# Optimization experiments

Hardware: AMD Instinct MI355X
Metric: run time of the kernel (lower is better)

## Reference

```python
import jax, jax.numpy as jnp
import numpy as np

B, N, M, C = 4, 2048, 576, 512
H, KVH, D = 8, 2, 64          # heads, kv heads, head_dim
E, TOPK, F = 8, 2, 2048       # experts, top-k, expert hidden (4*C)
EPS = 1e-6
NEG = -1e9


def setup_inputs() -> dict:
    key = jax.random.key(0)
    ks = iter(jax.random.split(key, 40))
    w = lambda shape, s=0.02: jax.random.normal(next(ks), shape, jnp.float32) * s
    d = {
        'x': jax.random.normal(next(ks), (B, N, C), jnp.float32),
        'vision_features': jax.random.normal(next(ks), (B, M, C), jnp.float32),
        'ln1_g': jnp.ones((C,), jnp.float32), 'ln1_b': jnp.zeros((C,), jnp.float32),
        'ln2_g': jnp.ones((C,), jnp.float32), 'ln2_b': jnp.zeros((C,), jnp.float32),
        'ln3_g': jnp.ones((C,), jnp.float32), 'ln3_b': jnp.zeros((C,), jnp.float32),
        # self-attention (GQA): q -> C, k/v -> KVH*D
        'sa_wq': w((C, C)), 'sa_bq': jnp.zeros((C,), jnp.float32),
        'sa_wk': w((C, KVH * D)), 'sa_bk': jnp.zeros((KVH * D,), jnp.float32),
        'sa_wv': w((C, KVH * D)), 'sa_bv': jnp.zeros((KVH * D,), jnp.float32),
        'sa_wo': w((C, C)), 'sa_bo': jnp.zeros((C,), jnp.float32),
        # cross-attention (GQA)
        'ca_wq': w((C, C)), 'ca_bq': jnp.zeros((C,), jnp.float32),
        'ca_wk': w((C, KVH * D)), 'ca_bk': jnp.zeros((KVH * D,), jnp.float32),
        'ca_wv': w((C, KVH * D)), 'ca_bv': jnp.zeros((KVH * D,), jnp.float32),
        'ca_wo': w((C, C)), 'ca_bo': jnp.zeros((C,), jnp.float32),
        # MoE: router + stacked expert MLPs (C -> F -> C, GELU)
        'router_w': w((C, E)), 'router_b': jnp.zeros((E,), jnp.float32),
        'e_w1': w((E, C, F)), 'e_b1': jnp.zeros((E, F), jnp.float32),
        'e_w2': w((E, F, C)), 'e_b2': jnp.zeros((E, C), jnp.float32),
    }
    return d


def _ln(x, g, b):
    mu = jnp.mean(x, -1, keepdims=True)
    var = jnp.mean(jnp.square(x - mu), -1, keepdims=True)
    return (x - mu) * jax.lax.rsqrt(var + EPS) * g + b


def _gqa_attn(xq, ctx, wq, bq, wk, bk, wv, bv, wo, bo, causal):
    b, n, c = xq.shape
    m = ctx.shape[1]
    q = (xq @ wq + bq).reshape(b, n, H, D).transpose(0, 2, 1, 3)      # bhnd
    k = (ctx @ wk + bk).reshape(b, m, KVH, D).transpose(0, 2, 1, 3)   # bgmd
    v = (ctx @ wv + bv).reshape(b, m, KVH, D).transpose(0, 2, 1, 3)
    rep = H // KVH
    k = jnp.repeat(k, rep, axis=1)  # repeat_interleave over head dim
    v = jnp.repeat(v, rep, axis=1)
    scores = jnp.einsum('bhnd,bhmd->bhnm', q, k) * (D ** -0.5)
    if causal:
        mask = jnp.tril(jnp.ones((n, m), bool))
        scores = jnp.where(mask, scores, NEG)
    a = jax.nn.softmax(scores, axis=-1)
    o = jnp.einsum('bhnm,bhmd->bhnd', a, v).transpose(0, 2, 1, 3).reshape(b, n, c)
    return o @ wo + bo


def _moe(x, router_w, router_b, e_w1, e_b1, e_w2, e_b2):
    logits = x @ router_w + router_b                    # [B,N,E]
    probs = jax.nn.softmax(logits, axis=-1)
    topv, topi = jax.lax.top_k(probs, TOPK)             # [B,N,K]
    topv = topv / jnp.sum(topv, -1, keepdims=True)      # renormalize top-k gates
    onehot = jax.nn.one_hot(topi, E, dtype=x.dtype)     # [B,N,K,E]
    gates = jnp.einsum('bnke,bnk->bne', onehot, topv)   # sparse gates, zeros off top-k
    h = jax.nn.gelu(jnp.einsum('bnc,ecf->bnef', x, e_w1) + e_b1)
    eo = jnp.einsum('bnef,efc->bnec', h, e_w2) + e_b2
    out = jnp.einsum('bne,bnec->bnc', gates, eo)
    # load-balance aux loss (Switch-style): E * sum_e f_e * P_e
    dispatch = jnp.sum(onehot, axis=2)                  # [B,N,E] routed mask
    f = jnp.mean(dispatch, axis=(0, 1))
    P = jnp.mean(probs, axis=(0, 1))
    aux = E * jnp.sum(f * P)
    return out, aux


def reference(x, vision_features,
              ln1_g, ln1_b, ln2_g, ln2_b, ln3_g, ln3_b,
              sa_wq, sa_bq, sa_wk, sa_bk, sa_wv, sa_bv, sa_wo, sa_bo,
              ca_wq, ca_bq, ca_wk, ca_bk, ca_wv, ca_bv, ca_wo, ca_bo,
              router_w, router_b, e_w1, e_b1, e_w2, e_b2):
    # pre-norm causal self-attn + residual
    h = _ln(x, ln1_g, ln1_b)
    x = x + _gqa_attn(h, h, sa_wq, sa_bq, sa_wk, sa_bk, sa_wv, sa_bv, sa_wo, sa_bo, True)
    # pre-norm cross-attn + residual
    h = _ln(x, ln2_g, ln2_b)
    x = x + _gqa_attn(h, vision_features, ca_wq, ca_bq, ca_wk, ca_bk, ca_wv, ca_bv, ca_wo, ca_bo, False)
    # pre-norm MoE FFN + residual
    h = _ln(x, ln3_g, ln3_b)
    m, aux = _moe(h, router_w, router_b, e_w1, e_b1, e_w2, e_b2)
    return x + m, aux
```

## Files before the change

kernel.cpp:

```cpp
#include <hip/hip_runtime.h>
#include <cstddef>
#include <cstdint>

#define B_   4
#define N_   2048
#define M_   576
#define C_   512
#define H_   8
#define KVH_ 2
#define D_   64
#define E_   8
#define F_   2048
#define BN_  (B_*N_)
#define BM_  (B_*M_)

typedef __attribute__((ext_vector_type(8))) short bf16x8;
typedef __attribute__((ext_vector_type(4))) float f32x4;

__device__ __forceinline__ unsigned short f2bf(float f) {
    union { float f; unsigned int u; } v; v.f = f;
    unsigned int r = v.u + 0x7FFFu + ((v.u >> 16) & 1u);
    return (unsigned short)(r >> 16);
}
__device__ __forceinline__ float bf2f(unsigned short u) {
    union { unsigned int u; float f; } v; v.u = ((unsigned int)u) << 16;
    return v.f;
}

typedef __attribute__((address_space(1))) void glb_void;
typedef __attribute__((address_space(3))) void lds_void;
__device__ __forceinline__ void gl2lds16(const unsigned short* g, unsigned short* l) {
    __builtin_amdgcn_global_load_lds((glb_void*)g, (lds_void*)l, 16, 0, 0);
}

__global__ __launch_bounds__(256) void ln_bf(const float* __restrict__ x,
    const float* __restrict__ g, const float* __restrict__ b, unsigned short* __restrict__ out)
{
    int row = blockIdx.x;
    const float* xr = x + (size_t)row * C_;
    float s = 0.f, ss = 0.f;
    for (int c = threadIdx.x; c < C_; c += 256) { float v = xr[c]; s += v; ss += v * v; }
    __shared__ float S1[256], S2[256];
    S1[threadIdx.x] = s; S2[threadIdx.x] = ss;
    __syncthreads();
    for (int o = 128; o > 0; o >>= 1) {
        if (threadIdx.x < o) { S1[threadIdx.x] += S1[threadIdx.x + o]; S2[threadIdx.x] += S2[threadIdx.x + o]; }
        __syncthreads();
    }
    float mu  = S1[0] * (1.f / C_);
    float var = S2[0] * (1.f / C_) - mu * mu;
    float inv = rsqrtf(var + 1e-6f);
    unsigned short* orow = out + (size_t)row * C_;
    for (int c = threadIdx.x; c < C_; c += 256)
        orow[c] = f2bf((xr[c] - mu) * inv * g[c] + b[c]);
}

__global__ __launch_bounds__(256) void ln_dual(const float* __restrict__ x,
    const float* __restrict__ g, const float* __restrict__ b,
    float* __restrict__ outF, unsigned short* __restrict__ outBf)
{
    int row = blockIdx.x;
    const float* xr = x + (size_t)row * C_;
    float s = 0.f, ss = 0.f;
    for (int c = threadIdx.x; c < C_; c += 256) { float v = xr[c]; s += v; ss += v * v; }
    __shared__ float S1[256], S2[256];
    S1[threadIdx.x] = s; S2[threadIdx.x] = ss;
    __syncthreads();
    for (int o = 128; o > 0; o >>= 1) {
        if (threadIdx.x < o) { S1[threadIdx.x] += S1[threadIdx.x + o]; S2[threadIdx.x] += S2[threadIdx.x + o]; }
        __syncthreads();
    }
    float mu  = S1[0] * (1.f / C_);
    float var = S2[0] * (1.f / C_) - mu * mu;
    float inv = rsqrtf(var + 1e-6f);
    for (int c = threadIdx.x; c < C_; c += 256) {
        float v = (xr[c] - mu) * inv * g[c] + b[c];
        outF[(size_t)row * C_ + c] = v;
        outBf[(size_t)row * C_ + c] = f2bf(v);
    }
}

__global__ __launch_bounds__(256) void cast_bf_kernel(const float* __restrict__ in,
    unsigned short* __restrict__ out)
{
    int i = (blockIdx.x * 256 + threadIdx.x) * 4;
    float4 v = *(const float4*)(in + i);
    ushort4 o;
    o.x = f2bf(v.x); o.y = f2bf(v.y); o.z = f2bf(v.z); o.w = f2bf(v.w);
    *(ushort4*)(out + i) = o;
}

__global__ __launch_bounds__(256) void transpose_cast(const float* __restrict__ Win,
    unsigned short* __restrict__ Wtout, int K, int N)
{
    const float* W = Win + (size_t)blockIdx.z * K * N;
    unsigned short* Wt = Wtout + (size_t)blockIdx.z * K * N;
    __shared__ float T[32][33];
    int tid = threadIdx.x;
    int r = tid >> 3, c4 = (tid & 7) * 4;
    int k0 = blockIdx.y * 32, n0 = blockIdx.x * 32;
    float4 v = *(const float4*)&W[(size_t)(k0 + r) * N + n0 + c4];
    T[r][c4 + 0] = v.x; T[r][c4 + 1] = v.y; T[r][c4 + 2] = v.z; T[r][c4 + 3] = v.w;
    __syncthreads();
    ushort4 o;
    o.x = f2bf(T[c4 + 0][r]); o.y = f2bf(T[c4 + 1][r]);
    o.z = f2bf(T[c4 + 2][r]); o.w = f2bf(T[c4 + 3][r]);
    *(ushort4*)&Wt[(size_t)(n0 + r) * K + k0 + c4] = o;
}

__global__ __launch_bounds__(256) void dense_mfma(
    const unsigned short* __restrict__ Abf,
    const unsigned short* __restrict__ Btbf,
    const float* __restrict__ bias,
    float* __restrict__ outF,
    unsigned short* __restrict__ outBf,
    unsigned short* __restrict__ outBf2,
    int N, int K, int mode, int NkPer)
{
    int row0 = blockIdx.y * 128;
    int col0 = blockIdx.x * 128;

    __shared__ unsigned short As[128 * 32];
    __shared__ unsigned short Bs[128 * 32];

    int tid = threadIdx.x;
    int lane = tid & 63, wid = tid >> 6;
    int lrow = lane >> 2;
    int cswz = (((lane & 3) ^ ((lane >> 3) & 3)) << 3);
    int ar0 = 16 * (wid * 2) + lrow;
    int ar1 = ar0 + 16;
    const unsigned short* gA0 = Abf + (size_t)(row0 + ar0) * K + cswz;
    const unsigned short* gA1 = Abf + (size_t)(row0 + ar1) * K + cswz;
    const unsigned short* gB0 = Btbf + (size_t)(col0 + ar0) * K + cswz;
    const unsigned short* gB1 = Btbf + (size_t)(col0 + ar1) * K + cswz;
    unsigned short* lA0 = As + (wid * 2) * 512;
    unsigned short* lA1 = lA0 + 512;
    unsigned short* lB0 = Bs + (wid * 2) * 512;
    unsigned short* lB1 = lB0 + 512;

    int wm0 = (wid & 1) * 64, wn0 = (wid >> 1) * 64;
    int lm = lane & 15, lq = lane >> 4;
    int swb = (lq ^ ((lm >> 1) & 3)) << 3;
    int aoff[4], boff[4];
#pragma unroll
    for (int i = 0; i < 4; i++) {
        aoff[i] = (wm0 + 16 * i + lm) * 32 + swb;
        boff[i] = (wn0 + 16 * i + lm) * 32 + swb;
    }

    f32x4 acc[4][4];
#pragma unroll
    for (int i = 0; i < 4; i++)
#pragma unroll
        for (int j = 0; j < 4; j++)
            acc[i][j] = (f32x4){0.f, 0.f, 0.f, 0.f};

    for (int k0 = 0; k0 < K; k0 += 32) {
        __syncthreads();
        gl2lds16(gA0 + k0, lA0);
        gl2lds16(gA1 + k0, lA1);
        gl2lds16(gB0 + k0, lB0);
        gl2lds16(gB1 + k0, lB1);
        __syncthreads();

        bf16x8 av[4], bv[4];
#pragma unroll
        for (int i = 0; i < 4; i++) av[i] = *(const bf16x8*)&As[aoff[i]];
#pragma unroll
        for (int i = 0; i < 4; i++) bv[i] = *(const bf16x8*)&Bs[boff[i]];
#pragma unroll
        for (int mi = 0; mi < 4; mi++)
#pragma unroll
            for (int ni = 0; ni < 4; ni++)
                acc[mi][ni] = __builtin_amdgcn_mfma_f32_16x16x32_bf16(av[mi], bv[ni], acc[mi][ni], 0, 0, 0);
    }

#pragma unroll
    for (int mi = 0; mi < 4; mi++) {
#pragma unroll
        for (int ri = 0; ri < 4; ri++) {
            int gr = row0 + wm0 + 16 * mi + lq * 4 + ri;
            if (mode == 3) {
#pragma unroll
                for (int ni = 0; ni < 4; ni++) {
                    int gc = col0 + wn0 + 16 * ni + lm;
                    float v = acc[mi][ni][ri] + bias[gc];
                    if (gc < 128) {
                        outBf[(size_t)gr * 128 + gc] = f2bf(v);
                    } else {
                        int bb = gr / NkPer;
                        int mm = gr - bb * NkPer;
                        outBf2[((size_t)bb * 128 + (gc - 128)) * NkPer + mm] = f2bf(v);
                    }
                }
            } else if (mode == 1) {
                size_t orow = (size_t)gr * N;
#pragma unroll
                for (int ni = 0; ni < 4; ni++) {
                    int gc = col0 + wn0 + 16 * ni + lm;
                    outF[orow + gc] += acc[mi][ni][ri] + bias[gc];
                }
            } else {
                size_t orow = (size_t)gr * N;
#pragma unroll
                for (int ni = 0; ni < 4; ni++) {
                    int gc = col0 + wn0 + 16 * ni + lm;
                    outBf[orow + gc] = f2bf(acc[mi][ni][ri] + bias[gc]);
                }
            }
        }
    }
}

__global__ __launch_bounds__(256) void attn_mfma(
    const unsigned short* __restrict__ Q,
    const unsigned short* __restrict__ K,
    const unsigned short* __restrict__ Vt,
    unsigned short* __restrict__ Obf,
    float* __restrict__ Opart,
    float* __restrict__ Lpart,
    int NkPer, int causal)
{
    __shared__ unsigned short Qs[64 * 72];
    __shared__ unsigned short Ks[64 * 72];
    __shared__ unsigned short Vs[64 * 72];
    unsigned short* Ps = Qs;

    int tid = threadIdx.x;
    int qt = blockIdx.x, bh = blockIdx.y, z = blockIdx.z;
    int b = bh >> 3, h = bh & 7, g = h >> 2;
    int q0 = qt * 64;

#pragma unroll
    for (int i = 0; i < 2; i++) {
        int s = tid + (i << 8);
        int r = s >> 3, c8 = (s & 7) << 3;
        *(uint4*)&Qs[r * 72 + c8] =
            *(const uint4*)&Q[(size_t)(b * N_ + q0 + r) * C_ + h * D_ + c8];
    }
    __syncthreads();

    int lane = tid & 63, wid = tid >> 6;
    int lm = lane & 15, lq = lane >> 4;
    int arow = wid * 16 + lm;

    bf16x8 qf[2];
    qf[0] = *(const bf16x8*)&Qs[arow * 72 + lq * 8];
    qf[1] = *(const bf16x8*)&Qs[arow * 72 + lq * 8 + 32];

    float lsum[4];
    f32x4 of[4];
#pragma unroll
    for (int i = 0; i < 4; i++) { lsum[i] = 0.f; of[i] = (f32x4){0.f,0.f,0.f,0.f}; }

    int nkt = causal ? (qt + 1) : ((NkPer + 63) >> 6);
    int nz = gridDim.z;
    int per = (nkt + nz - 1) / nz;
    int kt0 = z * per;
    int kt1 = min(nkt, kt0 + per);

    for (int kt = kt0; kt < kt1; kt++) {
        int k0 = kt << 6;
        __syncthreads();
#pragma unroll
        for (int i = 0; i < 2; i++) {
            int s = tid + (i << 8);
            int r = s >> 3, c8 = (s & 7) << 3;
            *(uint4*)&Ks[r * 72 + c8] =
                *(const uint4*)&K[(size_t)(b * NkPer + k0 + r) * (KVH_ * D_) + g * D_ + c8];
            *(uint4*)&Vs[r * 72 + c8] =
                *(const uint4*)&Vt[(size_t)(b * (KVH_ * D_) + g * D_ + r) * NkPer + k0 + c8];
        }
        __syncthreads();

        f32x4 sf[4];
#pragma unroll
        for (int i = 0; i < 4; i++) sf[i] = (f32x4){0.f,0.f,0.f,0.f};
#pragma unroll
        for (int ks = 0; ks < 2; ks++) {
#pragma unroll
            for (int ni = 0; ni < 4; ni++) {
                bf16x8 bv = *(const bf16x8*)&Ks[(16 * ni + lm) * 72 + lq * 8 + 32 * ks];
                sf[ni] = __builtin_amdgcn_mfma_f32_16x16x32_bf16(qf[ks], bv, sf[ni], 0, 0, 0);
            }
        }

        bool diag = causal && (k0 + 63 > q0 + wid * 16);
#pragma unroll
        for (int ni = 0; ni < 4; ni++)
#pragma unroll
            for (int ri = 0; ri < 4; ri++) {
                float v = sf[ni][ri] * 0.125f - 8.f;
                if (diag && (k0 + 16 * ni + lm > q0 + wid * 16 + lq * 4 + ri)) v = -1e30f;
                float p = __expf(v);
                sf[ni][ri] = p;
                lsum[ri] += p;
            }

#pragma unroll
        for (int ni = 0; ni < 4; ni++)
#pragma unroll
            for (int ri = 0; ri < 4; ri++)
                Ps[(wid * 16 + lq * 4 + ri) * 72 + 16 * ni + lm] = f2bf(sf[ni][ri]);
        __syncthreads();

        bf16x8 pf0 = *(const bf16x8*)&Ps[arow * 72 + lq * 8];
        bf16x8 pf1 = *(const bf16x8*)&Ps[arow * 72 + lq * 8 + 32];
#pragma unroll
        for (int ni = 0; ni < 4; ni++) {
            bf16x8 vv0 = *(const bf16x8*)&Vs[(16 * ni + lm) * 72 + lq * 8];
            bf16x8 vv1 = *(const bf16x8*)&Vs[(16 * ni + lm) * 72 + lq * 8 + 32];
            of[ni] = __builtin_amdgcn_mfma_f32_16x16x32_bf16(pf0, vv0, of[ni], 0, 0, 0);
            of[ni] = __builtin_amdgcn_mfma_f32_16x16x32_bf16(pf1, vv1, of[ni], 0, 0, 0);
        }
    }

#pragma unroll
    for (int ri = 0; ri < 4; ri++) {
        float s = lsum[ri];
        s += __shfl_xor(s, 1);
        s += __shfl_xor(s, 2);
        s += __shfl_xor(s, 4);
        s += __shfl_xor(s, 8);
        lsum[ri] = s;
    }

    if (nz == 1) {
#pragma unroll
        for (int ri = 0; ri < 4; ri++) {
            float inv = 1.f / lsum[ri];
            int q = q0 + wid * 16 + lq * 4 + ri;
            size_t orow = (size_t)(b * N_ + q) * C_ + h * D_;
#pragma unroll
            for (int ni = 0; ni < 4; ni++)
                Obf[orow + 16 * ni + lm] = f2bf(of[ni][ri] * inv);
        }
    } else {
        size_t zofs = (size_t)z * BN_ * C_;
#pragma unroll
        for (int ri = 0; ri < 4; ri++) {
            int q = q0 + wid * 16 + lq * 4 + ri;
            size_t orow = zofs + (size_t)(b * N_ + q) * C_ + h * D_;
#pragma unroll
            for (int ni = 0; ni < 4; ni++)
                Opart[orow + 16 * ni + lm] = of[ni][ri];
            if (lm == 0)
                Lpart[(size_t)z * (B_ * H_ * N_) + bh * N_ + q] = lsum[ri];
        }
    }
}

__global__ __launch_bounds__(256) void attn_combine(const float* __restrict__ Opart,
    const float* __restrict__ Lpart, unsigned short* __restrict__ Obf)
{
    int flat = (blockIdx.x * 256 + threadIdx.x) * 4;
    int row = flat >> 9, col = flat & 511;
    int b = row >> 11, q = row & (N_ - 1), h = col >> 6;
    int bh = b * 8 + h;
    float l = Lpart[bh * N_ + q] + Lpart[B_ * H_ * N_ + bh * N_ + q];
    float inv = 1.f / l;
    float4 o0 = *(const float4*)&Opart[flat];
    float4 o1 = *(const float4*)&Opart[(size_t)BN_ * C_ + flat];
    ushort4 o;
    o.x = f2bf((o0.x + o1.x) * inv); o.y = f2bf((o0.y + o1.y) * inv);
    o.z = f2bf((o0.z + o1.z) * inv); o.w = f2bf((o0.w + o1.w) * inv);
    *(ushort4*)&Obf[flat] = o;
}

__global__ __launch_bounds__(256) void router_logits(const float* __restrict__ X,
    const float* __restrict__ RW, const float* __restrict__ RB,
    float* __restrict__ gprobs, int* __restrict__ topi, float* __restrict__ gatesv)
{
    int lane = threadIdx.x & 63;
    int t = blockIdx.x * 4 + (threadIdx.x >> 6);
    const float* xr = X + (size_t)t * C_;
    float p[8] = {};
    for (int i = 0; i < 8; i++) {
        int c = i * 64 + lane;
        float xv = xr[c];
#pragma unroll
        for (int e = 0; e < 8; e++) p[e] = fmaf(xv, RW[c * 8 + e], p[e]);
    }
#pragma unroll
    for (int e = 0; e < 8; e++) {
        float v = p[e];
        v += __shfl_xor(v, 32, 64);
        v += __shfl_xor(v, 16, 64);
        v += __shfl_xor(v, 8, 64);
        v += __shfl_xor(v, 4, 64);
        v += __shfl_xor(v, 2, 64);
        v += __shfl_xor(v, 1, 64);
        p[e] = v;
    }
    if (lane == 0) {
        float logits[8], mx = -1e30f;
        for (int e = 0; e < 8; e++) { logits[e] = p[e] + RB[e]; mx = fmaxf(mx, logits[e]); }
        float pr[8], sum = 0.f;
        for (int e = 0; e < 8; e++) { pr[e] = expf(logits[e] - mx); sum += pr[e]; }
        float inv = 1.f / sum;
        for (int e = 0; e < 8; e++) { pr[e] *= inv; gprobs[t * 8 + e] = pr[e]; }
        int i1 = 0;
        for (int e = 1; e < 8; e++) if (pr[e] > pr[i1]) i1 = e;
        int i2 = (i1 == 0) ? 1 : 0;
        for (int e = 0; e < 8; e++) if (e != i1 && pr[e] > pr[i2]) i2 = e;
        float v1 = pr[i1], v2 = pr[i2], sg = 1.f / (v1 + v2);
        topi[t * 2]     = i1;  topi[t * 2 + 1]   = i2;
        gatesv[t * 2]   = v1 * sg;  gatesv[t * 2 + 1] = v2 * sg;
    }
}

__global__ __launch_bounds__(256) void router_reduce(const float* __restrict__ gprobs,
    const int* __restrict__ topi, int* __restrict__ ctrl, float* __restrict__ psum)
{
    __shared__ float fs[256];
    __shared__ int   is_[256];
    int bid = blockIdx.x, tid = threadIdx.x;
    if (bid < 8) {
        float s = 0.f;
        for (int t = tid; t < BN_; t += 256) s += gprobs[t * 8 + bid];
        fs[tid] = s; __syncthreads();
        for (int o = 128; o > 0; o >>= 1) { if (tid < o) fs[tid] += fs[tid + o]; __syncthreads(); }
        if (tid == 0) psum[bid] = fs[0];
    } else {
        int e = bid - 8, c = 0;
        for (int i = tid; i < BN_ * 2; i += 256) c += (topi[i] == e);
        is_[tid] = c; __syncthreads();
        for (int o = 128; o > 0; o >>= 1) { if (tid < o) is_[tid] += is_[tid + o]; __syncthreads(); }
        if (tid == 0) ctrl[e] = is_[0];
    }
}

__global__ void router_offsets(int* __restrict__ ctrl)
{
    if (threadIdx.x == 0 && blockIdx.x == 0) {
        int off = 0;
        for (int e = 0; e < 8; e++) {
            ctrl[16 + e] = off;
            off += (ctrl[e] + 127) & ~127;
        }
        ctrl[24] = off;
    }
}

__global__ __launch_bounds__(256) void router_scatter(const int* __restrict__ topi,
    const float* __restrict__ gatesv, int* __restrict__ rowtok,
    int* __restrict__ slotidx, int* __restrict__ ctrl)
{
    __shared__ int lcnt[8];
    __shared__ int lbase[8];
    int tid = threadIdx.x;
    int t = blockIdx.x * 256 + tid;
    if (tid < 8) lcnt[tid] = 0;
    __syncthreads();
    int e0 = topi[t * 2], e1 = topi[t * 2 + 1];
    int p0 = atomicAdd(&lcnt[e0], 1);
    int p1 = atomicAdd(&lcnt[e1], 1);
    __syncthreads();
    if (tid < 8) lbase[tid] = atomicAdd(&ctrl[8 + tid], lcnt[tid]);
    __syncthreads();
    int s0 = ctrl[16 + e0] + lbase[e0] + p0;
    int s1 = ctrl[16 + e1] + lbase[e1] + p1;
    rowtok[s0] = t;
    rowtok[s1] = t;
    slotidx[t * 2]     = s0;
    slotidx[t * 2 + 1] = s1;
}

__global__ __launch_bounds__(256) void moe_mfma(
    const unsigned short* __restrict__ Abf,
    const unsigned short* __restrict__ Btbf,
    const float* __restrict__ biasAll,
    unsigned short* __restrict__ outBf,
    const int* __restrict__ rowtok,
    const int* __restrict__ ctrl,
    int N, int K, int mode)
{
    int e = blockIdx.z;
    int cnt = ctrl[e];
    int row0 = blockIdx.y * 128;
    if (row0 >= cnt) return;
    int off = ctrl[16 + e];
    int col0 = blockIdx.x * 128;
    const unsigned short* Bt = Btbf + (size_t)e * N * K;
    const float* bias = biasAll + (size_t)e * N;

    __shared__ unsigned short As[128 * 32];
    __shared__ unsigned short Bs[128 * 32];
    __shared__ int toks[128];

    int tid = threadIdx.x;
    if (mode == 1 && tid < 128) {
        int gl = row0 + tid;
        toks[tid] = rowtok[off + (gl < cnt ? gl : 0)];
    }
    __syncthreads();

    int lane = tid & 63, wid = tid >> 6;
    int lrow = lane >> 2;
    int cswz = (((lane & 3) ^ ((lane >> 3) & 3)) << 3);
    int ar0 = 16 * (wid * 2) + lrow;
    int ar1 = ar0 + 16;
    const unsigned short *gA0, *gA1;
    if (mode == 1) {
        gA0 = Abf + (size_t)toks[ar0] * K + cswz;
        gA1 = Abf + (size_t)toks[ar1] * K + cswz;
    } else {
        gA0 = Abf + (size_t)(off + row0 + ar0) * K + cswz;
        gA1 = Abf + (size_t)(off + row0 + ar1) * K + cswz;
    }
    const unsigned short* gB0 = Bt + (size_t)(col0 + ar0) * K + cswz;
    const unsigned short* gB1 = Bt + (size_t)(col0 + ar1) * K + cswz;
    unsigned short* lA0 = As + (wid * 2) * 512;
    unsigned short* lA1 = lA0 + 512;
    unsigned short* lB0 = Bs + (wid * 2) * 512;
    unsigned short* lB1 = lB0 + 512;

    int wm0 = (wid & 1) * 64, wn0 = (wid >> 1) * 64;
    int lm = lane & 15, lq = lane >> 4;
    int swb = (lq ^ ((lm >> 1) & 3)) << 3;
    int aoff[4], boff[4];
#pragma unroll
    for (int i = 0; i < 4; i++) {
        aoff[i] = (wm0 + 16 * i + lm) * 32 + swb;
        boff[i] = (wn0 + 16 * i + lm) * 32 + swb;
    }

    f32x4 acc[4][4];
#pragma unroll
    for (int i = 0; i < 4; i++)
#pragma unroll
        for (int j = 0; j < 4; j++)
            acc[i][j] = (f32x4){0.f, 0.f, 0.f, 0.f};

    for (int k0 = 0; k0 < K; k0 += 32) {
        __syncthreads();
        gl2lds16(gA0 + k0, lA0);
        gl2lds16(gA1 + k0, lA1);
        gl2lds16(gB0 + k0, lB0);
        gl2lds16(gB1 + k0, lB1);
        __syncthreads();

        bf16x8 av[4], bv[4];
#pragma unroll
        for (int i = 0; i < 4; i++) av[i] = *(const bf16x8*)&As[aoff[i]];
#pragma unroll
        for (int i = 0; i < 4; i++) bv[i] = *(const bf16x8*)&Bs[boff[i]];
#pragma unroll
        for (int mi = 0; mi < 4; mi++)
#pragma unroll
            for (int ni = 0; ni < 4; ni++)
                acc[mi][ni] = __builtin_amdgcn_mfma_f32_16x16x32_bf16(av[mi], bv[ni], acc[mi][ni], 0, 0, 0);
    }

#pragma unroll
    for (int mi = 0; mi < 4; mi++) {
#pragma unroll
        for (int ri = 0; ri < 4; ri++) {
            int gl = row0 + wm0 + 16 * mi + lq * 4 + ri;
            size_t orow = (size_t)(off + gl) * N;
            if (mode == 1) {
#pragma unroll
                for (int ni = 0; ni < 4; ni++) {
                    int gc = col0 + wn0 + 16 * ni + lm;
                    float hv = 0.f;
                    if (gl < cnt) {
                        float xv = acc[mi][ni][ri] + bias[gc];
                        float z = 0.7978845608f * xv * fmaf(0.044715f, xv * xv, 1.f);
                        hv = __fdividef(xv, 1.f + __expf(-2.f * z));
                    }
                    outBf[orow + gc] = f2bf(hv);
                }
            } else {
#pragma unroll
                for (int ni = 0; ni < 4; ni++) {
                    int gc = col0 + wn0 + 16 * ni + lm;
                    outBf[orow + gc] = f2bf(acc[mi][ni][ri] + bias[gc]);
                }
            }
        }
    }
}

__global__ __launch_bounds__(256) void moe_combine(const unsigned short* __restrict__ slots,
    const int* __restrict__ slotidx, const float* __restrict__ gatesv,
    float* __restrict__ out)
{
    int flat = (blockIdx.x * 256 + threadIdx.x) * 4;
    int t = flat >> 9, c = flat & 511;
    int s0 = slotidx[t * 2], s1 = slotidx[t * 2 + 1];
    float g0 = gatesv[t * 2], g1 = gatesv[t * 2 + 1];
    ushort4 a = *(const ushort4*)&slots[(size_t)s0 * C_ + c];
    ushort4 b = *(const ushort4*)&slots[(size_t)s1 * C_ + c];
    float4 o = *(float4*)&out[flat];
    o.x += g0 * bf2f(a.x) + g1 * bf2f(b.x);
    o.y += g0 * bf2f(a.y) + g1 * bf2f(b.y);
    o.z += g0 * bf2f(a.z) + g1 * bf2f(b.z);
    o.w += g0 * bf2f(a.w) + g1 * bf2f(b.w);
    *(float4*)&out[flat] = o;
}

__global__ void aux_kernel(const int* __restrict__ ctrl, const float* __restrict__ psum,
                           float* __restrict__ outaux)
{
    if (threadIdx.x == 0 && blockIdx.x == 0) {
        float s = 0.f;
        for (int e = 0; e < 8; e++)
            s += ((float)ctrl[e] / (float)BN_) * (psum[e] / (float)BN_);
        outaux[0] = 8.f * s;
    }
}

extern "C" void kernel_launch(void* const* d_in, const int* in_sizes, int n_in,
                              void* d_out, int out_size, void* d_ws, size_t ws_size,
                              hipStream_t stream)
{
    const float* x      = (const float*)d_in[0];
    const float* vis    = (const float*)d_in[1];
    const float* ln1g   = (const float*)d_in[2];
    const float* ln1b   = (const float*)d_in[3];
    const float* ln2g   = (const float*)d_in[4];
    const float* ln2b   = (const float*)d_in[5];
    const float* ln3g   = (const float*)d_in[6];
    const float* ln3b   = (const float*)d_in[7];
    const float* sa_wq  = (const float*)d_in[8];
    const float* sa_bq  = (const float*)d_in[9];
    const float* sa_wk  = (const float*)d_in[10];
    const float* sa_bk  = (const float*)d_in[11];
    const float* sa_wv  = (const float*)d_in[12];
    const float* sa_bv  = (const float*)d_in[13];
    const float* sa_wo  = (const float*)d_in[14];
    const float* sa_bo  = (const float*)d_in[15];
    const float* ca_wq  = (const float*)d_in[16];
    const float* ca_bq  = (const float*)d_in[17];
    const float* ca_wk  = (const float*)d_in[18];
    const float* ca_bk  = (const float*)d_in[19];
    const float* ca_wv  = (const float*)d_in[20];
    const float* ca_bv  = (const float*)d_in[21];
    const float* ca_wo  = (const float*)d_in[22];
    const float* ca_bo  = (const float*)d_in[23];
    const float* rw     = (const float*)d_in[24];
    const float* rb     = (const float*)d_in[25];
    const float* e_w1   = (const float*)d_in[26];
    const float* e_b1   = (const float*)d_in[27];
    const float* e_w2   = (const float*)d_in[28];
    const float* e_b2   = (const float*)d_in[29];

    float* out = (float*)d_out;

    char* ws = (char*)d_ws;
    size_t off = 0;
    auto alloc = [&](size_t bytes) -> void* {
        void* p = ws + off;
        off = (off + bytes + 255) & ~(size_t)255;
        return p;
    };
    float* hbuf    = (float*)alloc((size_t)BN_ * C_ * 4);
    unsigned short* hbz = (unsigned short*)alloc((size_t)BN_ * C_ * 2);
    unsigned short* visbf = (unsigned short*)alloc((size_t)BM_ * C_ * 2);
    unsigned short* eoslots = (unsigned short*)hbuf;
    char* ureg = (char*)alloc((size_t)17408 * F_ * 2);
    unsigned short* moeH = (unsigned short*)ureg;
    unsigned short* qbf  = (unsigned short*)(ureg);
    unsigned short* obf  = (unsigned short*)(ureg + (size_t)BN_ * C_ * 2);
    unsigned short* kbf  = (unsigned short*)(ureg + (size_t)BN_ * C_ * 4);
    unsigned short* vtbf = (unsigned short*)(ureg + (size_t)BN_ * C_ * 4 + (size_t)BN_ * KVH_ * D_ * 2);
    float* opart = (float*)(ureg + (size_t)BN_ * C_ * 4 + (size_t)BN_ * KVH_ * D_ * 4);
    float* lpart = (float*)(ureg + (size_t)BN_ * C_ * 4 + (size_t)BN_ * KVH_ * D_ * 4
                                 + (size_t)2 * BN_ * C_ * 4);
    unsigned short* sa_wqt = (unsigned short*)alloc((size_t)C_ * C_ * 2);
    unsigned short* sa_wkvt = (unsigned short*)alloc((size_t)C_ * 2 * KVH_ * D_ * 2);
    unsigned short* sa_wot = (unsigned short*)alloc((size_t)C_ * C_ * 2);
    unsigned short* ca_wqt = (unsigned short*)alloc((size_t)C_ * C_ * 2);
    unsigned short* ca_wkvt = (unsigned short*)alloc((size_t)C_ * 2 * KVH_ * D_ * 2);
    unsigned short* ca_wot = (unsigned short*)alloc((size_t)C_ * C_ * 2);
    float* bkv_sa = (float*)alloc(256 * 4);
    float* bkv_ca = (float*)alloc(256 * 4);
    unsigned short* w1t  = (unsigned short*)alloc((size_t)E_ * C_ * F_ * 2);
    unsigned short* w2t  = (unsigned short*)alloc((size_t)E_ * F_ * C_ * 2);
    float* gprobs  = (float*)alloc((size_t)BN_ * 8 * 4);
    int*   topi    = (int*)  alloc((size_t)BN_ * 2 * 4);
    float* gatesv  = (float*)alloc((size_t)BN_ * 2 * 4);
    int*   rowtok  = (int*)  alloc(17408 * 4);
    int*   slotidx = (int*)  alloc((size_t)BN_ * 2 * 4);
    int*   ctrl    = (int*)  alloc(256);
    float* psum    = (float*)((char*)ctrl + 128);
    (void)ws_size; (void)in_sizes; (void)n_in; (void)out_size;

    hipMemcpyAsync(out, x, (size_t)BN_ * C_ * 4, hipMemcpyDeviceToDevice, stream);

    transpose_cast<<<dim3(16, 16, 1), 256, 0, stream>>>(sa_wq, sa_wqt, C_, C_);
    transpose_cast<<<dim3(4,  16, 1), 256, 0, stream>>>(sa_wk, sa_wkvt, C_, KVH_*D_);
    transpose_cast<<<dim3(4,  16, 1), 256, 0, stream>>>(sa_wv, sa_wkvt + 128 * C_, C_, KVH_*D_);
    transpose_cast<<<dim3(16, 16, 1), 256, 0, stream>>>(sa_wo, sa_wot, C_, C_);
    transpose_cast<<<dim3(16, 16, 1), 256, 0, stream>>>(ca_wq, ca_wqt, C_, C_);
    transpose_cast<<<dim3(4,  16, 1), 256, 0, stream>>>(ca_wk, ca_wkvt, C_, KVH_*D_);
    transpose_cast<<<dim3(4,  16, 1), 256, 0, stream>>>(ca_wv, ca_wkvt + 128 * C_, C_, KVH_*D_);
    transpose_cast<<<dim3(16, 16, 1), 256, 0, stream>>>(ca_wo, ca_wot, C_, C_);
    transpose_cast<<<dim3(F_/32, C_/32, E_), 256, 0, stream>>>(e_w1, w1t, C_, F_);
    transpose_cast<<<dim3(C_/32, F_/32, E_), 256, 0, stream>>>(e_w2, w2t, F_, C_);
    cast_bf_kernel<<<(BM_*C_)/1024, 256, 0, stream>>>(vis, visbf);
    hipMemcpyAsync(bkv_sa,       sa_bk, 128 * 4, hipMemcpyDeviceToDevice, stream);
    hipMemcpyAsync(bkv_sa + 128, sa_bv, 128 * 4, hipMemcpyDeviceToDevice, stream);
    hipMemcpyAsync(bkv_ca,       ca_bk, 128 * 4, hipMemcpyDeviceToDevice, stream);
    hipMemcpyAsync(bkv_ca + 128, ca_bv, 128 * 4, hipMemcpyDeviceToDevice, stream);

    ln_bf<<<BN_, 256, 0, stream>>>(out, ln1g, ln1b, hbz);
    dense_mfma<<<dim3(4, 64), 256, 0, stream>>>(hbz, sa_wqt, sa_bq, nullptr, qbf, nullptr, C_, C_, 0, 0);
    dense_mfma<<<dim3(2, 64), 256, 0, stream>>>(hbz, sa_wkvt, bkv_sa, nullptr, kbf, vtbf, 256, C_, 3, N_);
    attn_mfma<<<dim3(N_/64, B_*H_, 2), 256, 0, stream>>>(qbf, kbf, vtbf, nullptr, opart, lpart, N_, 1);
    attn_combine<<<(BN_*C_)/1024, 256, 0, stream>>>(opart, lpart, obf);
    dense_mfma<<<dim3(4, 64), 256, 0, stream>>>(obf, sa_wot, sa_bo, out, nullptr, nullptr, C_, C_, 1, 0);

    ln_bf<<<BN_, 256, 0, stream>>>(out, ln2g, ln2b, hbz);
    dense_mfma<<<dim3(4, 64), 256, 0, stream>>>(hbz, ca_wqt, ca_bq, nullptr, qbf, nullptr, C_, C_, 0, 0);
    dense_mfma<<<dim3(2, 18), 256, 0, stream>>>(visbf, ca_wkvt, bkv_ca, nullptr, kbf, vtbf, 256, C_, 3, M_);
    attn_mfma<<<dim3(N_/64, B_*H_, 1), 256, 0, stream>>>(qbf, kbf, vtbf, obf, nullptr, nullptr, M_, 0);
    dense_mfma<<<dim3(4, 64), 256, 0, stream>>>(obf, ca_wot, ca_bo, out, nullptr, nullptr, C_, C_, 1, 0);

    ln_dual<<<BN_, 256, 0, stream>>>(out, ln3g, ln3b, hbuf, hbz);
    hipMemsetAsync(ctrl, 0, 256, stream);
    router_logits<<<BN_/4, 256, 0, stream>>>(hbuf, rw, rb, gprobs, topi, gatesv);
    router_reduce<<<16, 256, 0, stream>>>(gprobs, topi, ctrl, psum);
    router_offsets<<<1, 1, 0, stream>>>(ctrl);
    router_scatter<<<BN_/256, 256, 0, stream>>>(topi, gatesv, rowtok, slotidx, ctrl);
    moe_mfma<<<dim3(F_/128, BN_/128, E_), 256, 0, stream>>>(
        hbz, w1t, e_b1, moeH, rowtok, ctrl, F_, C_, 1);
    moe_mfma<<<dim3(C_/128, BN_/128, E_), 256, 0, stream>>>(
        moeH, w2t, e_b2, eoslots, rowtok, ctrl, C_, F_, 2);
    moe_combine<<<(BN_*C_)/1024, 256, 0, stream>>>(eoslots, slotidx, gatesv, out);
    aux_kernel<<<1, 1, 0, stream>>>(ctrl, psum, out + (size_t)BN_ * C_);
}
```

Before: 698.2 us.

## Merge prep kernels, fuse residual copy, reorder MoE grid, stage MoE stores via LDS

All weight transpose-casts, the vision cast, the bias copies and the ctrl reset now run in one prep kernel, replacing about sixteen separate launches and memcpys. The initial copy of x into the output is dropped; the first output projection writes x + proj directly through a new epilogue mode. The MoE GEMM grid swaps its x/y axes so row tiles vary fastest, and its epilogue stages bf16 results in LDS so global stores become 16-byte vectors. These changes target launch overhead, one full-activation copy and scattered narrow stores, at the cost of extra LDS use in the MoE kernel, which may lower occupancy.

```diff
diff --git a/kernel.cpp b/kernel.cpp
--- a/kernel.cpp
+++ b/kernel.cpp
@@ -33,6 +33,74 @@
     __builtin_amdgcn_global_load_lds((glb_void*)g, (lds_void*)l, 16, 0, 0);
 }
 
+__global__ __launch_bounds__(256) void prep_all(
+    const float* __restrict__ sa_wq, const float* __restrict__ sa_wk,
+    const float* __restrict__ sa_wv, const float* __restrict__ sa_wo,
+    const float* __restrict__ ca_wq, const float* __restrict__ ca_wk,
+    const float* __restrict__ ca_wv, const float* __restrict__ ca_wo,
+    const float* __restrict__ e_w1, const float* __restrict__ e_w2,
+    const float* __restrict__ vis,
+    const float* __restrict__ sa_bk, const float* __restrict__ sa_bv,
+    const float* __restrict__ ca_bk, const float* __restrict__ ca_bv,
+    unsigned short* __restrict__ sa_wqt, unsigned short* __restrict__ sa_wkvt,
+    unsigned short* __restrict__ sa_wot,
+    unsigned short* __restrict__ ca_wqt, unsigned short* __restrict__ ca_wkvt,
+    unsigned short* __restrict__ ca_wot,
+    unsigned short* __restrict__ w1t, unsigned short* __restrict__ w2t,
+    unsigned short* __restrict__ visbf,
+    float* __restrict__ bkv_sa, float* __restrict__ bkv_ca,
+    int* __restrict__ ctrl)
+{
+    __shared__ float T[32][33];
+    int t = blockIdx.x;
+    int tid = threadIdx.x;
+
+    if (t < 17664) {
+        const float* W; unsigned short* Wt; int K, N, kt, nt;
+        if (t < 1280) {
+            if (t < 256)      { W = sa_wq; Wt = sa_wqt; K = 512; N = 512; int r = t;        nt = r & 15; kt = r >> 4; }
+            else if (t < 320) { W = sa_wk; Wt = sa_wkvt;            K = 512; N = 128; int r = t - 256; nt = r & 3;  kt = r >> 2; }
+            else if (t < 384) { W = sa_wv; Wt = sa_wkvt + 128*512;  K = 512; N = 128; int r = t - 320; nt = r & 3;  kt = r >> 2; }
+            else if (t < 640) { W = sa_wo; Wt = sa_wot; K = 512; N = 512; int r = t - 384;  nt = r & 15; kt = r >> 4; }
+            else if (t < 896) { W = ca_wq; Wt = ca_wqt; K = 512; N = 512; int r = t - 640;  nt = r & 15; kt = r >> 4; }
+            else if (t < 960) { W = ca_wk; Wt = ca_wkvt;            K = 512; N = 128; int r = t - 896; nt = r & 3;  kt = r >> 2; }
+            else if (t < 1024){ W = ca_wv; Wt = ca_wkvt + 128*512;  K = 512; N = 128; int r = t - 960; nt = r & 3;  kt = r >> 2; }
+            else              { W = ca_wo; Wt = ca_wot; K = 512; N = 512; int r = t - 1024; nt = r & 15; kt = r >> 4; }
+        } else if (t < 9472) {
+            int r = t - 1280; int e = r >> 10; r &= 1023;
+            W = e_w1 + (size_t)e * C_ * F_; Wt = w1t + (size_t)e * C_ * F_;
+            K = C_; N = F_; nt = r & 63; kt = r >> 6;
+        } else {
+            int r = t - 9472; int e = r >> 10; r &= 1023;
+            W = e_w2 + (size_t)e * F_ * C_; Wt = w2t + (size_t)e * F_ * C_;
+            K = F_; N = C_; nt = r & 15; kt = r >> 4;
+        }
+        int rr = tid >> 3, c4 = (tid & 7) * 4;
+        int k0 = kt * 32, n0 = nt * 32;
+        float4 v = *(const float4*)&W[(size_t)(k0 + rr) * N + n0 + c4];
+        T[rr][c4 + 0] = v.x; T[rr][c4 + 1] = v.y; T[rr][c4 + 2] = v.z; T[rr][c4 + 3] = v.w;
+        __syncthreads();
+        ushort4 o;
+        o.x = f2bf(T[c4 + 0][rr]); o.y = f2bf(T[c4 + 1][rr]);
+        o.z = f2bf(T[c4 + 2][rr]); o.w = f2bf(T[c4 + 3][rr]);
+        *(ushort4*)&Wt[(size_t)(n0 + rr) * K + k0 + c4] = o;
+    } else if (t < 18816) {
+        int i = (t - 17664) * 1024 + tid * 4;
+        float4 v = *(const float4*)(vis + i);
+        ushort4 o;
+        o.x = f2bf(v.x); o.y = f2bf(v.y); o.z = f2bf(v.z); o.w = f2bf(v.w);
+        *(ushort4*)(visbf + i) = o;
+    } else {
+        if (tid < 128) {
+            bkv_sa[tid]       = sa_bk[tid];
+            bkv_sa[128 + tid] = sa_bv[tid];
+            bkv_ca[tid]       = ca_bk[tid];
+            bkv_ca[128 + tid] = ca_bv[tid];
+        }
+        if (tid < 32) ctrl[tid] = 0;
+    }
+}
+
 __global__ __launch_bounds__(256) void ln_bf(const float* __restrict__ x,
     const float* __restrict__ g, const float* __restrict__ b, unsigned short* __restrict__ out)
 {
@@ -80,38 +148,11 @@
     }
 }
 
-__global__ __launch_bounds__(256) void cast_bf_kernel(const float* __restrict__ in,
-    unsigned short* __restrict__ out)
-{
-    int i = (blockIdx.x * 256 + threadIdx.x) * 4;
-    float4 v = *(const float4*)(in + i);
-    ushort4 o;
-    o.x = f2bf(v.x); o.y = f2bf(v.y); o.z = f2bf(v.z); o.w = f2bf(v.w);
-    *(ushort4*)(out + i) = o;
-}
-
-__global__ __launch_bounds__(256) void transpose_cast(const float* __restrict__ Win,
-    unsigned short* __restrict__ Wtout, int K, int N)
-{
-    const float* W = Win + (size_t)blockIdx.z * K * N;
-    unsigned short* Wt = Wtout + (size_t)blockIdx.z * K * N;
-    __shared__ float T[32][33];
-    int tid = threadIdx.x;
-    int r = tid >> 3, c4 = (tid & 7) * 4;
-    int k0 = blockIdx.y * 32, n0 = blockIdx.x * 32;
-    float4 v = *(const float4*)&W[(size_t)(k0 + r) * N + n0 + c4];
-    T[r][c4 + 0] = v.x; T[r][c4 + 1] = v.y; T[r][c4 + 2] = v.z; T[r][c4 + 3] = v.w;
-    __syncthreads();
-    ushort4 o;
-    o.x = f2bf(T[c4 + 0][r]); o.y = f2bf(T[c4 + 1][r]);
-    o.z = f2bf(T[c4 + 2][r]); o.w = f2bf(T[c4 + 3][r]);
-    *(ushort4*)&Wt[(size_t)(n0 + r) * K + k0 + c4] = o;
-}
-
 __global__ __launch_bounds__(256) void dense_mfma(
     const unsigned short* __restrict__ Abf,
     const unsigned short* __restrict__ Btbf,
     const float* __restrict__ bias,
+    const float* __restrict__ xin,
     float* __restrict__ outF,
     unsigned short* __restrict__ outBf,
     unsigned short* __restrict__ outBf2,
@@ -199,6 +240,13 @@
                 for (int ni = 0; ni < 4; ni++) {
                     int gc = col0 + wn0 + 16 * ni + lm;
                     outF[orow + gc] += acc[mi][ni][ri] + bias[gc];
+                }
+            } else if (mode == 4) {
+                size_t orow = (size_t)gr * N;
+#pragma unroll
+                for (int ni = 0; ni < 4; ni++) {
+                    int gc = col0 + wn0 + 16 * ni + lm;
+                    outF[orow + gc] = xin[orow + gc] + acc[mi][ni][ri] + bias[gc];
                 }
             } else {
                 size_t orow = (size_t)gr * N;
@@ -477,15 +525,16 @@
 {
     int e = blockIdx.z;
     int cnt = ctrl[e];
-    int row0 = blockIdx.y * 128;
+    int row0 = blockIdx.x * 128;
     if (row0 >= cnt) return;
     int off = ctrl[16 + e];
-    int col0 = blockIdx.x * 128;
+    int col0 = blockIdx.y * 128;
     const unsigned short* Bt = Btbf + (size_t)e * N * K;
     const float* bias = biasAll + (size_t)e * N;
 
     __shared__ unsigned short As[128 * 32];
     __shared__ unsigned short Bs[128 * 32];
+    __shared__ __align__(16) unsigned short Cs[4][32 * 72];
     __shared__ int toks[128];
 
     int tid = threadIdx.x;
@@ -552,32 +601,39 @@
                 acc[mi][ni] = __builtin_amdgcn_mfma_f32_16x16x32_bf16(av[mi], bv[ni], acc[mi][ni], 0, 0, 0);
     }
 
-#pragma unroll
-    for (int mi = 0; mi < 4; mi++) {
-#pragma unroll
-        for (int ri = 0; ri < 4; ri++) {
-            int gl = row0 + wm0 + 16 * mi + lq * 4 + ri;
-            size_t orow = (size_t)(off + gl) * N;
-            if (mode == 1) {
+    unsigned short* cs = Cs[wid];
+#pragma unroll
+    for (int p = 0; p < 2; p++) {
+#pragma unroll
+        for (int m2 = 0; m2 < 2; m2++) {
+            int mi = 2 * p + m2;
+#pragma unroll
+            for (int ri = 0; ri < 4; ri++) {
+                int gl = row0 + wm0 + 16 * mi + lq * 4 + ri;
+                bool valid = gl < cnt;
 #pragma unroll
                 for (int ni = 0; ni < 4; ni++) {
                     int gc = col0 + wn0 + 16 * ni + lm;
-                    float hv = 0.f;
-                    if (gl < cnt) {
-                        float xv = acc[mi][ni][ri] + bias[gc];
+                    float xv = acc[mi][ni][ri] + bias[gc];
+                    float hv;
+                    if (mode == 1) {
                         float z = 0.7978845608f * xv * fmaf(0.044715f, xv * xv, 1.f);
-                        hv = __fdividef(xv, 1.f + __expf(-2.f * z));
+                        hv = valid ? __fdividef(xv, 1.f + __expf(-2.f * z)) : 0.f;
+                    } else {
+                        hv = xv;
                     }
-                    outBf[orow + gc] = f2bf(hv);
-                }
-            } else {
-#pragma unroll
-                for (int ni = 0; ni < 4; ni++) {
-                    int gc = col0 + wn0 + 16 * ni + lm;
-                    outBf[orow + gc] = f2bf(acc[mi][ni][ri] + bias[gc]);
+                    cs[(m2 * 16 + lq * 4 + ri) * 72 + 16 * ni + lm] = f2bf(hv);
                 }
             }
         }
+        int rr = lane >> 1;
+        int ch = (lane & 1) * 32;
+        int gl2 = row0 + wm0 + 32 * p + rr;
+        size_t orow = (size_t)(off + gl2) * N + col0 + wn0 + ch;
+        const unsigned short* rsrc = &cs[rr * 72 + ch];
+#pragma unroll
+        for (int j = 0; j < 4; j++)
+            *(uint4*)&outBf[orow + j * 8] = *(const uint4*)&rsrc[j * 8];
     }
 }
 
@@ -686,46 +742,33 @@
     float* psum    = (float*)((char*)ctrl + 128);
     (void)ws_size; (void)in_sizes; (void)n_in; (void)out_size;
 
-    hipMemcpyAsync(out, x, (size_t)BN_ * C_ * 4, hipMemcpyDeviceToDevice, stream);
-
-    transpose_cast<<<dim3(16, 16, 1), 256, 0, stream>>>(sa_wq, sa_wqt, C_, C_);
-    transpose_cast<<<dim3(4,  16, 1), 256, 0, stream>>>(sa_wk, sa_wkvt, C_, KVH_*D_);
-    transpose_cast<<<dim3(4,  16, 1), 256, 0, stream>>>(sa_wv, sa_wkvt + 128 * C_, C_, KVH_*D_);
-    transpose_cast<<<dim3(16, 16, 1), 256, 0, stream>>>(sa_wo, sa_wot, C_, C_);
-    transpose_cast<<<dim3(16, 16, 1), 256, 0, stream>>>(ca_wq, ca_wqt, C_, C_);
-    transpose_cast<<<dim3(4,  16, 1), 256, 0, stream>>>(ca_wk, ca_wkvt, C_, KVH_*D_);
-    transpose_cast<<<dim3(4,  16, 1), 256, 0, stream>>>(ca_wv, ca_wkvt + 128 * C_, C_, KVH_*D_);
-    transpose_cast<<<dim3(16, 16, 1), 256, 0, stream>>>(ca_wo, ca_wot, C_, C_);
-    transpose_cast<<<dim3(F_/32, C_/32, E_), 256, 0, stream>>>(e_w1, w1t, C_, F_);
-    transpose_cast<<<dim3(C_/32, F_/32, E_), 256, 0, stream>>>(e_w2, w2t, F_, C_);
-    cast_bf_kernel<<<(BM_*C_)/1024, 256, 0, stream>>>(vis, visbf);
-    hipMemcpyAsync(bkv_sa,       sa_bk, 128 * 4, hipMemcpyDeviceToDevice, stream);
-    hipMemcpyAsync(bkv_sa + 128, sa_bv, 128 * 4, hipMemcpyDeviceToDevice, stream);
-    hipMemcpyAsync(bkv_ca,       ca_bk, 128 * 4, hipMemcpyDeviceToDevice, stream);
-    hipMemcpyAsync(bkv_ca + 128, ca_bv, 128 * 4, hipMemcpyDeviceToDevice, stream);
-
-    ln_bf<<<BN_, 256, 0, stream>>>(out, ln1g, ln1b, hbz);
-    dense_mfma<<<dim3(4, 64), 256, 0, stream>>>(hbz, sa_wqt, sa_bq, nullptr, qbf, nullptr, C_, C_, 0, 0);
-    dense_mfma<<<dim3(2, 64), 256, 0, stream>>>(hbz, sa_wkvt, bkv_sa, nullptr, kbf, vtbf, 256, C_, 3, N_);
+    prep_all<<<18817, 256, 0, stream>>>(
+        sa_wq, sa_wk, sa_wv, sa_wo, ca_wq, ca_wk, ca_wv, ca_wo,
+        e_w1, e_w2, vis, sa_bk, sa_bv, ca_bk, ca_bv,
+        sa_wqt, sa_wkvt, sa_wot, ca_wqt, ca_wkvt, ca_wot,
+        w1t, w2t, visbf, bkv_sa, bkv_ca, ctrl);
+
+    ln_bf<<<BN_, 256, 0, stream>>>(x, ln1g, ln1b, hbz);
+    dense_mfma<<<dim3(4, 64), 256, 0, stream>>>(hbz, sa_wqt, sa_bq, nullptr, nullptr, qbf, nullptr, C_, C_, 0, 0);
+    dense_mfma<<<dim3(2, 64), 256, 0, stream>>>(hbz, sa_wkvt, bkv_sa, nullptr, nullptr, kbf, vtbf, 256, C_, 3, N_);
     attn_mfma<<<dim3(N_/64, B_*H_, 2), 256, 0, stream>>>(qbf, kbf, vtbf, nullptr, opart, lpart, N_, 1);
     attn_combine<<<(BN_*C_)/1024, 256, 0, stream>>>(opart, lpart, obf);
-    dense_mfma<<<dim3(4, 64), 256, 0, stream>>>(obf, sa_wot, sa_bo, out, nullptr, nullptr, C_, C_, 1, 0);
+    dense_mfma<<<dim3(4, 64), 256, 0, stream>>>(obf, sa_wot, sa_bo, x, out, nullptr, nullptr, C_, C_, 4, 0);
 
     ln_bf<<<BN_, 256, 0, stream>>>(out, ln2g, ln2b, hbz);
-    dense_mfma<<<dim3(4, 64), 256, 0, stream>>>(hbz, ca_wqt, ca_bq, nullptr, qbf, nullptr, C_, C_, 0, 0);
-    dense_mfma<<<dim3(2, 18), 256, 0, stream>>>(visbf, ca_wkvt, bkv_ca, nullptr, kbf, vtbf, 256, C_, 3, M_);
+    dense_mfma<<<dim3(4, 64), 256, 0, stream>>>(hbz, ca_wqt, ca_bq, nullptr, nullptr, qbf, nullptr, C_, C_, 0, 0);
+    dense_mfma<<<dim3(2, 18), 256, 0, stream>>>(visbf, ca_wkvt, bkv_ca, nullptr, nullptr, kbf, vtbf, 256, C_, 3, M_);
     attn_mfma<<<dim3(N_/64, B_*H_, 1), 256, 0, stream>>>(qbf, kbf, vtbf, obf, nullptr, nullptr, M_, 0);
-    dense_mfma<<<dim3(4, 64), 256, 0, stream>>>(obf, ca_wot, ca_bo, out, nullptr, nullptr, C_, C_, 1, 0);
+    dense_mfma<<<dim3(4, 64), 256, 0, stream>>>(obf, ca_wot, ca_bo, nullptr, out, nullptr, nullptr, C_, C_, 1, 0);
 
     ln_dual<<<BN_, 256, 0, stream>>>(out, ln3g, ln3b, hbuf, hbz);
-    hipMemsetAsync(ctrl, 0, 256, stream);
     router_logits<<<BN_/4, 256, 0, stream>>>(hbuf, rw, rb, gprobs, topi, gatesv);
     router_reduce<<<16, 256, 0, stream>>>(gprobs, topi, ctrl, psum);
     router_offsets<<<1, 1, 0, stream>>>(ctrl);
     router_scatter<<<BN_/256, 256, 0, stream>>>(topi, gatesv, rowtok, slotidx, ctrl);
-    moe_mfma<<<dim3(F_/128, BN_/128, E_), 256, 0, stream>>>(
+    moe_mfma<<<dim3(BN_/128, F_/128, E_), 256, 0, stream>>>(
         hbz, w1t, e_b1, moeH, rowtok, ctrl, F_, C_, 1);
-    moe_mfma<<<dim3(C_/128, BN_/128, E_), 256, 0, stream>>>(
+    moe_mfma<<<dim3(BN_/128, C_/128, E_), 256, 0, stream>>>(
         moeH, w2t, e_b2, eoslots, rowtok, ctrl, C_, F_, 2);
     moe_combine<<<(BN_*C_)/1024, 256, 0, stream>>>(eoslots, slotidx, gatesv, out);
     aux_kernel<<<1, 1, 0, stream>>>(ctrl, psum, out + (size_t)BN_ * C_);
```

Result: slower. 729.7 us (+4.5%).
